# Performance work log

Hardware: AMD Instinct MI355X
Metric: run time of the kernel (lower is better)

## Reference

```python
import jax, jax.numpy as jnp
import numpy as np

B, D, L = 4, 64, 4096  # batch, pos feature dim (=pos_learnable_dim), sequence length

def setup_inputs() -> dict:
    key = jax.random.key(0)
    k1, k2 = jax.random.split(key, 2)
    pos_embed = jax.random.normal(k1, (B, D, L), dtype=jnp.float32)
    # _LinearWithBias(D, D): torch weight [out, in], bias [out]
    W_pos = (jax.random.normal(k2, (D, D), dtype=jnp.float32) / np.float32(np.sqrt(D)))
    b_pos = jnp.zeros((D,), dtype=jnp.float32)
    SOFTPLUS0 = 0.6931472  # softplus(0) = ln 2, gpytorch default raw param -> constrained value
    lengthscale = jnp.asarray(SOFTPLUS0, dtype=jnp.float32)   # RBFKernel lengthscale
    outputscale = jnp.asarray(SOFTPLUS0, dtype=jnp.float32)   # ScaleKernel outputscale
    return {"pos_embed": pos_embed, "W_pos": W_pos, "b_pos": b_pos,
            "lengthscale": lengthscale, "outputscale": outputscale}

def reference(pos_embed, W_pos, b_pos, lengthscale, outputscale):
    # pos_embed: [B, D, L]
    x = jnp.swapaxes(pos_embed, 1, 2)          # [B, L, D] (transpose, linear, transpose back, transpose again)
    x = x @ W_pos.T + b_pos                    # learnable positional linear on feature dim
    # gpytorch ScaleKernel(RBFKernel): outputscale * exp(-0.5 * ||(x_i - x_j)/lengthscale||^2)
    xs = x / lengthscale                       # [B, L, D]
    sq = jnp.sum(xs * xs, axis=-1)             # [B, L]
    sq_dist = sq[:, :, None] + sq[:, None, :] - 2.0 * jnp.einsum('bld,bmd->blm', xs, xs)
    sq_dist = jnp.maximum(sq_dist, 0.0)        # gpytorch clamps sq dist at 0
    return outputscale * jnp.exp(-0.5 * sq_dist)  # [B, L, L]
```

## Files before the change

### kernel.cpp

```cpp
#include <hip/hip_runtime.h>

using bf16x8 = __attribute__((ext_vector_type(8))) __bf16;
using f32x16 = __attribute__((ext_vector_type(16))) float;

#define BB 4
#define DD 64
#define LL 4096

__global__ __launch_bounds__(256) void prep_kernel(
    const float* __restrict__ pe,
    const float* __restrict__ W,
    const float* __restrict__ bias,
    const float* __restrict__ ls,
    __bf16* __restrict__ xs,
    float* __restrict__ h)
{
    __shared__ float pe_lds[DD][64];
    __shared__ float W_lds[DD * DD];
    __shared__ float hpart[4][64];

    const int tid = threadIdx.x;
    const int blk = blockIdx.x;
    const int b  = blk >> 6;
    const int l0 = (blk & 63) * 64;

    {
        const int l = tid & 63;
        const int kb = tid >> 6;
        #pragma unroll
        for (int it = 0; it < 16; ++it) {
            const int k = it * 4 + kb;
            pe_lds[k][l] = pe[((size_t)b * DD + k) * LL + l0 + l];
        }
    }
    #pragma unroll
    for (int it = 0; it < 16; ++it)
        W_lds[it * 256 + tid] = W[it * 256 + tid];
    __syncthreads();

    const int w = tid >> 6;
    const int l = tid & 63;
    const float SQRT_LOG2E = 1.2011224087864498f;
    const float scale = SQRT_LOG2E / ls[0];

    float acc[16];
    #pragma unroll
    for (int i = 0; i < 16; ++i) acc[i] = bias[w * 16 + i];

    for (int k4 = 0; k4 < 16; ++k4) {
        const float p0 = pe_lds[k4 * 4 + 0][l];
        const float p1 = pe_lds[k4 * 4 + 1][l];
        const float p2 = pe_lds[k4 * 4 + 2][l];
        const float p3 = pe_lds[k4 * 4 + 3][l];
        #pragma unroll
        for (int i = 0; i < 16; ++i) {
            const float4 wv = *(const float4*)&W_lds[(w * 16 + i) * DD + k4 * 4];
            acc[i] += p0 * wv.x + p1 * wv.y + p2 * wv.z + p3 * wv.w;
        }
    }

    unsigned short out16[16];
    float hs = 0.0f;
    #pragma unroll
    for (int i = 0; i < 16; ++i) {
        const float xf = acc[i] * scale;
        const __bf16 bv = (__bf16)xf;
        const float xr = (float)bv;
        hs += xr * xr;
        out16[i] = __builtin_bit_cast(unsigned short, bv);
    }
    {
        __bf16* dst = xs + ((size_t)b * LL + l0 + l) * DD + w * 16;
        *(uint4*)dst       = *(const uint4*)&out16[0];
        *(uint4*)(dst + 8) = *(const uint4*)&out16[8];
    }
    hpart[w][l] = hs;
    __syncthreads();
    if (tid < 64) {
        const float s = hpart[0][tid] + hpart[1][tid] + hpart[2][tid] + hpart[3][tid];
        h[(size_t)b * LL + tid + l0] = 0.5f * s;
    }
}

__global__ __launch_bounds__(256) void gram_kernel(
    const __bf16* __restrict__ xs,
    const float* __restrict__ h,
    const float* __restrict__ osc,
    float* __restrict__ out)
{
    const int bid = blockIdx.x;
    const int b  = bid >> 10;
    const int t  = bid & 1023;
    const int ti = t >> 3;
    const int tj = t & 7;

    const int tid  = threadIdx.x;
    const int wid  = tid >> 6;
    const int lane = tid & 63;
    const int lr = lane & 31, lg = lane >> 5;

    const int rows0 = ti * 32;
    const int cols0 = tj * 512 + wid * 128;

    const __bf16* xsb = xs + (size_t)b * LL * DD;
    const float*  hb  = h + (size_t)b * LL;

    const float c  = osc[0];
    const float lc = __builtin_log2f(c);

    bf16x8 af[4], bg[4][4];
    #pragma unroll
    for (int kk = 0; kk < 4; ++kk)
        af[kk] = *(const bf16x8*)(xsb + (size_t)(rows0 + lr) * DD + kk * 16 + lg * 8);
    #pragma unroll
    for (int nt = 0; nt < 4; ++nt)
        #pragma unroll
        for (int kk = 0; kk < 4; ++kk)
            bg[nt][kk] = *(const bf16x8*)(xsb + (size_t)(cols0 + nt * 32 + lr) * DD + kk * 16 + lg * 8);

    f32x16 acc[4];
    #pragma unroll
    for (int nt = 0; nt < 4; ++nt) acc[nt] = (f32x16)(0.0f);

    #pragma unroll
    for (int kk = 0; kk < 4; ++kk)
        #pragma unroll
        for (int nt = 0; nt < 4; ++nt)
            acc[nt] = __builtin_amdgcn_mfma_f32_32x32x16_bf16(af[kk], bg[nt][kk], acc[nt], 0, 0, 0);

    float hi2[16];
    #pragma unroll
    for (int r = 0; r < 16; ++r)
        hi2[r] = hb[rows0 + (r & 3) + 8 * (r >> 2) + 4 * lg] - lc;

    #pragma unroll
    for (int nt = 0; nt < 4; ++nt) {
        const int col = cols0 + nt * 32 + lr;
        const float hj = hb[col];
        float* op = out + ((size_t)b * LL + rows0 + 4 * lg) * LL + col;
        #pragma unroll
        for (int r = 0; r < 16; ++r) {
            float tt = acc[nt][r] - hi2[r] - hj;
            tt = fminf(tt, lc);
            const int rowoff = (r & 3) + 8 * (r >> 2);
            op[(size_t)rowoff * LL] = __builtin_amdgcn_exp2f(tt);
        }
    }
}

extern "C" void kernel_launch(void* const* d_in, const int* in_sizes, int n_in,
                              void* d_out, int out_size, void* d_ws, size_t ws_size,
                              hipStream_t stream) {
    const float* pe   = (const float*)d_in[0];
    const float* W    = (const float*)d_in[1];
    const float* bias = (const float*)d_in[2];
    const float* ls   = (const float*)d_in[3];
    const float* osc  = (const float*)d_in[4];
    float* out = (float*)d_out;

    __bf16* xs = (__bf16*)d_ws;
    float*  h  = (float*)((char*)d_ws + (size_t)BB * LL * DD * 2);

    prep_kernel<<<256, 256, 0, stream>>>(pe, W, bias, ls, xs, h);
    gram_kernel<<<BB * 32 * 32, 256, 0, stream>>>(xs, h, osc, out);
}
```

Before: 68.43 us.

## Enlarge gram tiles per block, double-buffer B fragments, use nontemporal stores

The gram kernel now gives each block a 128x512 output tile instead of 32x512, so there are four times fewer blocks. Each wave computes a 64-row by 4x64-column region, reusing its A fragments across four column steps. B fragments are double-buffered so the next column step's loads overlap the current MFMAs and exp epilogue. Output writes become nontemporal stores to avoid polluting cache with the 256MB output. The cost is more registers per wave and fewer blocks, which may reduce occupancy.

```diff
diff --git a/kernel.cpp b/kernel.cpp
--- a/kernel.cpp
+++ b/kernel.cpp
@@ -89,18 +89,18 @@
     float* __restrict__ out)
 {
     const int bid = blockIdx.x;
-    const int b  = bid >> 10;
-    const int t  = bid & 1023;
+    const int b  = bid >> 8;
+    const int t  = bid & 255;
     const int ti = t >> 3;
-    const int tj = t & 7;
+    const int tg = t & 7;
 
     const int tid  = threadIdx.x;
     const int wid  = tid >> 6;
     const int lane = tid & 63;
     const int lr = lane & 31, lg = lane >> 5;
 
-    const int rows0 = ti * 32;
-    const int cols0 = tj * 512 + wid * 128;
+    const int rows0 = ti * 128 + (wid >> 1) * 64;
+    const int colw  = tg * 512 + (wid & 1) * 64;
 
     const __bf16* xsb = xs + (size_t)b * LL * DD;
     const float*  hb  = h + (size_t)b * LL;
@@ -108,44 +108,82 @@
     const float c  = osc[0];
     const float lc = __builtin_log2f(c);
 
-    bf16x8 af[4], bg[4][4];
-    #pragma unroll
-    for (int kk = 0; kk < 4; ++kk)
-        af[kk] = *(const bf16x8*)(xsb + (size_t)(rows0 + lr) * DD + kk * 16 + lg * 8);
-    #pragma unroll
-    for (int nt = 0; nt < 4; ++nt)
+    bf16x8 af[2][4];
+    #pragma unroll
+    for (int mt = 0; mt < 2; ++mt)
         #pragma unroll
         for (int kk = 0; kk < 4; ++kk)
-            bg[nt][kk] = *(const bf16x8*)(xsb + (size_t)(cols0 + nt * 32 + lr) * DD + kk * 16 + lg * 8);
-
-    f32x16 acc[4];
-    #pragma unroll
-    for (int nt = 0; nt < 4; ++nt) acc[nt] = (f32x16)(0.0f);
-
-    #pragma unroll
-    for (int kk = 0; kk < 4; ++kk)
-        #pragma unroll
-        for (int nt = 0; nt < 4; ++nt)
-            acc[nt] = __builtin_amdgcn_mfma_f32_32x32x16_bf16(af[kk], bg[nt][kk], acc[nt], 0, 0, 0);
-
-    float hi2[16];
-    #pragma unroll
-    for (int r = 0; r < 16; ++r)
-        hi2[r] = hb[rows0 + (r & 3) + 8 * (r >> 2) + 4 * lg] - lc;
-
-    #pragma unroll
-    for (int nt = 0; nt < 4; ++nt) {
-        const int col = cols0 + nt * 32 + lr;
-        const float hj = hb[col];
-        float* op = out + ((size_t)b * LL + rows0 + 4 * lg) * LL + col;
-        #pragma unroll
-        for (int r = 0; r < 16; ++r) {
-            float tt = acc[nt][r] - hi2[r] - hj;
-            tt = fminf(tt, lc);
-            const int rowoff = (r & 3) + 8 * (r >> 2);
-            op[(size_t)rowoff * LL] = __builtin_amdgcn_exp2f(tt);
-        }
-    }
+            af[mt][kk] = *(const bf16x8*)(xsb + (size_t)(rows0 + mt * 32 + lr) * DD + kk * 16 + lg * 8);
+
+    float hi2[2][16];
+    #pragma unroll
+    for (int mt = 0; mt < 2; ++mt)
+        #pragma unroll
+        for (int r = 0; r < 16; ++r)
+            hi2[mt][r] = hb[rows0 + mt * 32 + (r & 3) + 8 * (r >> 2) + 4 * lg] - lc;
+
+    float hj[4][2];
+    #pragma unroll
+    for (int s = 0; s < 4; ++s)
+        #pragma unroll
+        for (int nt = 0; nt < 2; ++nt)
+            hj[s][nt] = hb[colw + s * 128 + nt * 32 + lr];
+
+    bf16x8 bgA[2][4], bgB[2][4];
+
+#define LOADBG(BUF, S)                                                         \
+    _Pragma("unroll")                                                          \
+    for (int nt = 0; nt < 2; ++nt)                                             \
+        _Pragma("unroll")                                                      \
+        for (int kk = 0; kk < 4; ++kk)                                         \
+            BUF[nt][kk] = *(const bf16x8*)(xsb +                               \
+                (size_t)(colw + (S) * 128 + nt * 32 + lr) * DD + kk * 16 + lg * 8);
+
+#define MFMA_EPI(BUF, S)                                                       \
+    {                                                                          \
+        f32x16 acc[2][2];                                                      \
+        _Pragma("unroll")                                                      \
+        for (int mt = 0; mt < 2; ++mt)                                         \
+            _Pragma("unroll")                                                  \
+            for (int nt = 0; nt < 2; ++nt)                                     \
+                acc[mt][nt] = (f32x16)(0.0f);                                  \
+        _Pragma("unroll")                                                      \
+        for (int kk = 0; kk < 4; ++kk)                                         \
+            _Pragma("unroll")                                                  \
+            for (int mt = 0; mt < 2; ++mt)                                     \
+                _Pragma("unroll")                                              \
+                for (int nt = 0; nt < 2; ++nt)                                 \
+                    acc[mt][nt] = __builtin_amdgcn_mfma_f32_32x32x16_bf16(     \
+                        af[mt][kk], BUF[nt][kk], acc[mt][nt], 0, 0, 0);        \
+        _Pragma("unroll")                                                      \
+        for (int mt = 0; mt < 2; ++mt) {                                       \
+            _Pragma("unroll")                                                  \
+            for (int nt = 0; nt < 2; ++nt) {                                   \
+                const int col = colw + (S) * 128 + nt * 32 + lr;               \
+                float* op = out + ((size_t)b * LL + rows0 + mt * 32 + 4 * lg) * LL + col; \
+                _Pragma("unroll")                                              \
+                for (int r = 0; r < 16; ++r) {                                 \
+                    float tt = acc[mt][nt][r] - hi2[mt][r] - hj[S][nt];        \
+                    tt = fminf(tt, lc);                                        \
+                    const int rowoff = (r & 3) + 8 * (r >> 2);                 \
+                    __builtin_nontemporal_store(__builtin_amdgcn_exp2f(tt),    \
+                                                &op[(size_t)rowoff * LL]);     \
+                }                                                              \
+            }                                                                  \
+        }                                                                      \
+    }
+
+    LOADBG(bgA, 0)
+    LOADBG(bgB, 1)
+    MFMA_EPI(bgA, 0)
+    LOADBG(bgA, 2)
+    MFMA_EPI(bgB, 1)
+    LOADBG(bgB, 3)
+    MFMA_EPI(bgA, 2)
+    MFMA_EPI(bgB, 3)
+
+#undef LOADBG
+#undef MFMA_EPI
 }
 
 extern "C" void kernel_launch(void* const* d_in, const int* in_sizes, int n_in,
@@ -162,5 +200,5 @@
     float*  h  = (float*)((char*)d_ws + (size_t)BB * LL * DD * 2);
 
     prep_kernel<<<256, 256, 0, stream>>>(pe, W, bias, ls, xs, h);
-    gram_kernel<<<BB * 32 * 32, 256, 0, stream>>>(xs, h, osc, out);
+    gram_kernel<<<BB * 32 * 8, 256, 0, stream>>>(xs, h, osc, out);
 }
```

Measured after the change: 76.59 us. +11.9%, slower.
